# Kernel tuning notes

Hardware: AMD Instinct MI355X
Metric: run time of the kernel (lower is better)

## Reference

```python
import jax, jax.numpy as jnp
import numpy as np

B, C, H, W, O, K = 8, 3, 512, 512, 64, 9


def conv2d(x, w, b):
    # 3x3, stride 1, padding 1, NCHW/OIHW
    y = jax.lax.conv_general_dilated(
        x, w, window_strides=(1, 1), padding=[(1, 1), (1, 1)],
        dimension_numbers=('NCHW', 'OIHW', 'NCHW'))
    return y + b[None, :, None, None]


def setup_inputs() -> dict:
    key = jax.random.key(0)
    ks = jax.random.split(key, 6)
    x = jax.random.normal(ks[0], (B, C, H, W), jnp.float32)
    w_simple = jax.random.normal(ks[1], (O, C, 3, 3), jnp.float32) * 0.1
    w_off = jax.random.normal(ks[2], (2 * K, C, 3, 3), jnp.float32) * 0.05
    b_off = jax.random.normal(ks[3], (2 * K,), jnp.float32) * 0.1
    w_mask = jax.random.normal(ks[4], (K, C, 3, 3), jnp.float32) * 0.1
    b_mask = jax.random.normal(ks[5], (K,), jnp.float32) * 0.1
    return {'x': x, 'w_simple': w_simple, 'w_off': w_off, 'b_off': b_off,
            'w_mask': w_mask, 'b_mask': b_mask}


def deform_conv2d(x, offset, mask, weight):
    # x: [B,C,H,W]; offset: [B,2K,H,W] (dy,dx interleaved per tap);
    # mask: [B,K,H,W]; weight: [O,C,3,3]; stride 1, pad 1, dilation 1.
    off = offset.reshape(B, K, 2, H, W)
    dy, dx = off[:, :, 0], off[:, :, 1]          # [B,K,H,W]
    ki = (jnp.arange(K) // 3).astype(x.dtype)[None, :, None, None]
    kj = (jnp.arange(K) % 3).astype(x.dtype)[None, :, None, None]
    hh = jnp.arange(H, dtype=x.dtype)[None, None, :, None]
    ww = jnp.arange(W, dtype=x.dtype)[None, None, None, :]
    py = hh - 1.0 + ki + dy                       # sampling rows [B,K,H,W]
    px = ww - 1.0 + kj + dx                       # sampling cols [B,K,H,W]

    y0f = jnp.floor(py); x0f = jnp.floor(px)
    ty = py - y0f; tx = px - x0f                  # bilinear fractions
    y0 = y0f.astype(jnp.int32); x0 = x0f.astype(jnp.int32)

    def gather(yi, xi):
        # zero-padded gather of x at integer coords yi, xi -> [B,C,K,H,W]
        valid = ((yi >= 0) & (yi < H) & (xi >= 0) & (xi < W))
        yc = jnp.clip(yi, 0, H - 1)
        xc = jnp.clip(xi, 0, W - 1)
        lin = yc * W + xc                         # [B,K,H,W]
        def per_b(xb, linb):
            return xb.reshape(C, -1)[:, linb.reshape(-1)].reshape(C, K, H, W)
        vals = jax.vmap(per_b)(x, lin)
        return vals * valid[:, None].astype(x.dtype)

    v = (gather(y0, x0) * ((1 - ty) * (1 - tx))[:, None]
         + gather(y0, x0 + 1) * ((1 - ty) * tx)[:, None]
         + gather(y0 + 1, x0) * (ty * (1 - tx))[:, None]
         + gather(y0 + 1, x0 + 1) * (ty * tx)[:, None])  # [B,C,K,H,W]
    v = v * mask[:, None]                          # modulated samples
    return jnp.einsum('ock,bckhw->bohw', weight.reshape(O, C, K), v)


def reference(x, w_simple, w_off, b_off, w_mask, b_mask):
    offset = conv2d(x, w_off, b_off)
    mask = jax.nn.sigmoid(conv2d(x, w_mask, b_mask))
    return deform_conv2d(x, offset, mask, w_simple)
```

## Files before the change

### kernel.cpp

```cpp
#include <hip/hip_runtime.h>

#define BB 8
#define CC 3
#define HH 512
#define WW 512
#define OO 64
#define KK 9

__global__ __launch_bounds__(256, 4) void fused_deform_kernel(
    const float* __restrict__ x,
    const float* __restrict__ w_simple,
    const float* __restrict__ w_off,
    const float* __restrict__ b_off,
    const float* __restrict__ w_mask,
    const float* __restrict__ b_mask,
    float* __restrict__ out)
{
    __shared__ __align__(16) float s_woff[18 * 28];
    __shared__ __align__(16) float s_wmsk[9 * 28];
    __shared__ __align__(16) float s_w[64 * 28];
    __shared__ float s_boff[18];
    __shared__ float s_bmsk[9];

    const int tid = threadIdx.x;
    for (int t = tid; t < 18 * 28; t += 256) { int j = t / 28, i = t % 28; s_woff[t] = (i < 27) ? w_off[j * 27 + i] : 0.f; }
    for (int t = tid; t < 9 * 28; t += 256)  { int j = t / 28, i = t % 28; s_wmsk[t] = (i < 27) ? w_mask[j * 27 + i] : 0.f; }
    for (int t = tid; t < 64 * 28; t += 256) { int j = t / 28, i = t % 28; s_w[t]    = (i < 27) ? w_simple[j * 27 + i] : 0.f; }
    if (tid < 18) s_boff[tid] = b_off[tid];
    if (tid < 9)  s_bmsk[tid] = b_mask[tid];
    __syncthreads();

    const int bid = blockIdx.x;
    const int nbid = (bid & 7) * 1024 + (bid >> 3);

    const int idx = nbid * 256 + tid;
    const int w = idx & (WW - 1);
    const int h = (idx >> 9) & (HH - 1);
    const int b = idx >> 18;

    const float* xb = x + (size_t)b * CC * HH * WW;

    float nb[28];
    #pragma unroll
    for (int c = 0; c < CC; ++c) {
        const float* xc = xb + c * HH * WW;
        #pragma unroll
        for (int i = 0; i < 9; ++i) {
            int yy = h - 1 + i / 3;
            int xx = w - 1 + i % 3;
            float v = 0.f;
            if ((unsigned)yy < (unsigned)HH && (unsigned)xx < (unsigned)WW)
                v = xc[yy * WW + xx];
            nb[c * 9 + i] = v;
        }
    }
    nb[27] = 0.f;

    float offv[18];
    #pragma unroll
    for (int j = 0; j < 18; ++j) {
        float acc = s_boff[j];
        const float4* wp = (const float4*)(s_woff + j * 28);
        #pragma unroll
        for (int q = 0; q < 7; ++q) {
            float4 wq = wp[q];
            acc = fmaf(wq.x, nb[q * 4 + 0], acc);
            acc = fmaf(wq.y, nb[q * 4 + 1], acc);
            acc = fmaf(wq.z, nb[q * 4 + 2], acc);
            acc = fmaf(wq.w, nb[q * 4 + 3], acc);
        }
        offv[j] = acc;
    }

    float mval[9];
    #pragma unroll
    for (int j = 0; j < 9; ++j) {
        float acc = s_bmsk[j];
        const float4* wp = (const float4*)(s_wmsk + j * 28);
        #pragma unroll
        for (int q = 0; q < 7; ++q) {
            float4 wq = wp[q];
            acc = fmaf(wq.x, nb[q * 4 + 0], acc);
            acc = fmaf(wq.y, nb[q * 4 + 1], acc);
            acc = fmaf(wq.z, nb[q * 4 + 2], acc);
            acc = fmaf(wq.w, nb[q * 4 + 3], acc);
        }
        mval[j] = 1.f / (1.f + __expf(-acc));
    }

    float vv[28];
    vv[27] = 0.f;
    #pragma unroll
    for (int k = 0; k < 9; ++k) {
        float py = (float)(h - 1 + k / 3) + offv[2 * k + 0];
        float px = (float)(w - 1 + k % 3) + offv[2 * k + 1];
        float y0f = floorf(py);
        float x0f = floorf(px);
        float ty = py - y0f;
        float tx = px - x0f;
        int y0 = (int)y0f;
        int x0 = (int)x0f;
        int y1 = y0 + 1;
        int x1 = x0 + 1;
        bool vy0 = (unsigned)y0 < (unsigned)HH;
        bool vy1 = (unsigned)y1 < (unsigned)HH;
        bool vx0 = (unsigned)x0 < (unsigned)WW;
        bool vx1 = (unsigned)x1 < (unsigned)WW;
        int yc0 = min(max(y0, 0), HH - 1);
        int yc1 = min(max(y1, 0), HH - 1);
        int xc0 = min(max(x0, 0), WW - 1);
        int xc1 = min(max(x1, 0), WW - 1);
        int l00 = yc0 * WW + xc0;
        int l01 = yc0 * WW + xc1;
        int l10 = yc1 * WW + xc0;
        int l11 = yc1 * WW + xc1;
        float mk = mval[k];
        float w00 = (vy0 && vx0) ? (1.f - ty) * (1.f - tx) * mk : 0.f;
        float w01 = (vy0 && vx1) ? (1.f - ty) * tx * mk : 0.f;
        float w10 = (vy1 && vx0) ? ty * (1.f - tx) * mk : 0.f;
        float w11 = (vy1 && vx1) ? ty * tx * mk : 0.f;
        #pragma unroll
        for (int c = 0; c < CC; ++c) {
            const float* xc = xb + c * HH * WW;
            float s;
            s = w00 * xc[l00];
            s = fmaf(w01, xc[l01], s);
            s = fmaf(w10, xc[l10], s);
            s = fmaf(w11, xc[l11], s);
            vv[c * 9 + k] = s;
        }
    }

    const size_t obase = (size_t)b * OO * HH * WW + (size_t)h * WW + w;
    #pragma unroll 4
    for (int o = 0; o < OO; ++o) {
        float acc = 0.f;
        const float4* wp = (const float4*)(s_w + o * 28);
        #pragma unroll
        for (int q = 0; q < 7; ++q) {
            float4 wq = wp[q];
            acc = fmaf(wq.x, vv[q * 4 + 0], acc);
            acc = fmaf(wq.y, vv[q * 4 + 1], acc);
            acc = fmaf(wq.z, vv[q * 4 + 2], acc);
            acc = fmaf(wq.w, vv[q * 4 + 3], acc);
        }
        __builtin_nontemporal_store(acc, &out[obase + (size_t)o * HH * WW]);
    }
}

extern "C" void kernel_launch(void* const* d_in, const int* in_sizes, int n_in,
                              void* d_out, int out_size, void* d_ws, size_t ws_size,
                              hipStream_t stream) {
    const float* x        = (const float*)d_in[0];
    const float* w_simple = (const float*)d_in[1];
    const float* w_off    = (const float*)d_in[2];
    const float* b_off    = (const float*)d_in[3];
    const float* w_mask   = (const float*)d_in[4];
    const float* b_mask   = (const float*)d_in[5];
    float* out = (float*)d_out;

    const int total = BB * HH * WW;
    const int block = 256;
    const int grid = total / block;
    fused_deform_kernel<<<grid, block, 0, stream>>>(x, w_simple, w_off, b_off, w_mask, b_mask, out);
}
```

Before: 660.2 us.

## Compute output channel contraction with split-bf16 MFMA via per-wave LDS staging

Replaces the per-thread scalar 64x27 FMA loop for the final output projection with MFMA 16x16x32 bf16 instructions. Both weights and sampled values are split into hi/lo bf16 pairs, and three MFMAs approximate fp32 accuracy. Per-pixel samples are staged through per-wave LDS so they can be rearranged into the MFMA operand layout. The change also swaps the sigmoid divide for a hardware reciprocal and lowers launch bounds to account for the added LDS and register use. The split-bf16 scheme drops the lo*lo term, which slightly reduces precision, and the added LDS traffic costs some occupancy.

```diff
diff --git a/kernel.cpp b/kernel.cpp
--- a/kernel.cpp
+++ b/kernel.cpp
@@ -1,4 +1,7 @@
 #include <hip/hip_runtime.h>
+
+typedef __attribute__((ext_vector_type(8))) short bf8v;
+typedef __attribute__((ext_vector_type(4))) float f4v;
 
 #define BB 8
 #define CC 3
@@ -6,8 +9,20 @@
 #define WW 512
 #define OO 64
 #define KK 9
-
-__global__ __launch_bounds__(256, 4) void fused_deform_kernel(
+#define HW (HH * WW)
+#define VBSTRIDE 176
+
+static __device__ __forceinline__ unsigned short f2bf(float f) {
+    unsigned u = __builtin_bit_cast(unsigned, f);
+    unsigned r = u + 0x7fffu + ((u >> 16) & 1u);
+    return (unsigned short)(r >> 16);
+}
+static __device__ __forceinline__ float bf2f(unsigned short h) {
+    unsigned u = ((unsigned)h) << 16;
+    return __builtin_bit_cast(float, u);
+}
+
+__global__ __launch_bounds__(256, 3) void fused_deform_kernel(
     const float* __restrict__ x,
     const float* __restrict__ w_simple,
     const float* __restrict__ w_off,
@@ -18,16 +33,36 @@
 {
     __shared__ __align__(16) float s_woff[18 * 28];
     __shared__ __align__(16) float s_wmsk[9 * 28];
-    __shared__ __align__(16) float s_w[64 * 28];
     __shared__ float s_boff[18];
     __shared__ float s_bmsk[9];
+    __shared__ __align__(16) unsigned char s_vb[4 * 64 * VBSTRIDE];
 
     const int tid = threadIdx.x;
+    const int lane = tid & 63;
+    const int wv = tid >> 6;
+
     for (int t = tid; t < 18 * 28; t += 256) { int j = t / 28, i = t % 28; s_woff[t] = (i < 27) ? w_off[j * 27 + i] : 0.f; }
     for (int t = tid; t < 9 * 28; t += 256)  { int j = t / 28, i = t % 28; s_wmsk[t] = (i < 27) ? w_mask[j * 27 + i] : 0.f; }
-    for (int t = tid; t < 64 * 28; t += 256) { int j = t / 28, i = t % 28; s_w[t]    = (i < 27) ? w_simple[j * 27 + i] : 0.f; }
     if (tid < 18) s_boff[tid] = b_off[tid];
     if (tid < 9)  s_bmsk[tid] = b_mask[tid];
+
+    bf8v wh[4], wl[4];
+    {
+        const int row = lane & 15;
+        const int ko = (lane >> 4) * 8;
+        #pragma unroll
+        for (int m = 0; m < 4; ++m) {
+            const float* ws = w_simple + (size_t)(m * 16 + row) * 27 + ko;
+            #pragma unroll
+            for (int j = 0; j < 8; ++j) {
+                float f = (ko + j < 27) ? ws[j] : 0.f;
+                unsigned short hh = f2bf(f);
+                unsigned short ll = f2bf(f - bf2f(hh));
+                wh[m][j] = (short)hh;
+                wl[m][j] = (short)ll;
+            }
+        }
+    }
     __syncthreads();
 
     const int bid = blockIdx.x;
@@ -38,12 +73,12 @@
     const int h = (idx >> 9) & (HH - 1);
     const int b = idx >> 18;
 
-    const float* xb = x + (size_t)b * CC * HH * WW;
+    const float* xb = x + (size_t)b * CC * HW;
 
     float nb[28];
     #pragma unroll
     for (int c = 0; c < CC; ++c) {
-        const float* xc = xb + c * HH * WW;
+        const float* xc = xb + c * HW;
         #pragma unroll
         for (int i = 0; i < 9; ++i) {
             int yy = h - 1 + i / 3;
@@ -85,11 +120,10 @@
             acc = fmaf(wq.z, nb[q * 4 + 2], acc);
             acc = fmaf(wq.w, nb[q * 4 + 3], acc);
         }
-        mval[j] = 1.f / (1.f + __expf(-acc));
-    }
-
-    float vv[28];
-    vv[27] = 0.f;
+        mval[j] = __builtin_amdgcn_rcpf(1.f + __expf(-acc));
+    }
+
+    float vv[27];
     #pragma unroll
     for (int k = 0; k < 9; ++k) {
         float py = (float)(h - 1 + k / 3) + offv[2 * k + 0];
@@ -121,7 +155,7 @@
         float w11 = (vy1 && vx1) ? ty * tx * mk : 0.f;
         #pragma unroll
         for (int c = 0; c < CC; ++c) {
-            const float* xc = xb + c * HH * WW;
+            const float* xc = xb + c * HW;
             float s;
             s = w00 * xc[l00];
             s = fmaf(w01, xc[l01], s);
@@ -131,20 +165,51 @@
         }
     }
 
-    const size_t obase = (size_t)b * OO * HH * WW + (size_t)h * WW + w;
-    #pragma unroll 4
-    for (int o = 0; o < OO; ++o) {
-        float acc = 0.f;
-        const float4* wp = (const float4*)(s_w + o * 28);
-        #pragma unroll
-        for (int q = 0; q < 7; ++q) {
-            float4 wq = wp[q];
-            acc = fmaf(wq.x, vv[q * 4 + 0], acc);
-            acc = fmaf(wq.y, vv[q * 4 + 1], acc);
-            acc = fmaf(wq.z, vv[q * 4 + 2], acc);
-            acc = fmaf(wq.w, vv[q * 4 + 3], acc);
-        }
-        __builtin_nontemporal_store(acc, &out[obase + (size_t)o * HH * WW]);
+    unsigned char* vb = s_vb + wv * (64 * VBSTRIDE);
+    {
+        unsigned hiw[16], low[16];
+        #pragma unroll
+        for (int i = 0; i < 16; ++i) {
+            float a = (2 * i < 27) ? vv[2 * i] : 0.f;
+            float c2 = (2 * i + 1 < 27) ? vv[2 * i + 1] : 0.f;
+            unsigned short ha = f2bf(a), hb = f2bf(c2);
+            unsigned short la = f2bf(a - bf2f(ha)), lb = f2bf(c2 - bf2f(hb));
+            hiw[i] = (unsigned)ha | ((unsigned)hb << 16);
+            low[i] = (unsigned)la | ((unsigned)lb << 16);
+        }
+        uint4* dh = (uint4*)(vb + lane * VBSTRIDE);
+        dh[0] = make_uint4(hiw[0], hiw[1], hiw[2], hiw[3]);
+        dh[1] = make_uint4(hiw[4], hiw[5], hiw[6], hiw[7]);
+        dh[2] = make_uint4(hiw[8], hiw[9], hiw[10], hiw[11]);
+        dh[3] = make_uint4(hiw[12], hiw[13], hiw[14], hiw[15]);
+        uint4* dl = (uint4*)(vb + lane * VBSTRIDE + 64);
+        dl[0] = make_uint4(low[0], low[1], low[2], low[3]);
+        dl[1] = make_uint4(low[4], low[5], low[6], low[7]);
+        dl[2] = make_uint4(low[8], low[9], low[10], low[11]);
+        dl[3] = make_uint4(low[12], low[13], low[14], low[15]);
+    }
+    asm volatile("s_waitcnt lgkmcnt(0)" ::: "memory");
+
+    const int wavecol = ((nbid & 1) << 8) + wv * 64;
+    const int kb16 = (lane >> 4) * 16;
+    float* obase = out + (size_t)b * OO * HW + (size_t)h * WW;
+    #pragma unroll
+    for (int g = 0; g < 4; ++g) {
+        const unsigned char* rs = vb + (size_t)(g * 16 + (lane & 15)) * VBSTRIDE + kb16;
+        bf8v bh = *(const bf8v*)rs;
+        bf8v bl = *(const bf8v*)(rs + 64);
+        float* op0 = obase + (wavecol + g * 16 + (lane & 15));
+        #pragma unroll
+        for (int m = 0; m < 4; ++m) {
+            f4v acc = {0.f, 0.f, 0.f, 0.f};
+            acc = __builtin_amdgcn_mfma_f32_16x16x32_bf16(wh[m], bl, acc, 0, 0, 0);
+            acc = __builtin_amdgcn_mfma_f32_16x16x32_bf16(wl[m], bh, acc, 0, 0, 0);
+            acc = __builtin_amdgcn_mfma_f32_16x16x32_bf16(wh[m], bh, acc, 0, 0, 0);
+            const int o0 = m * 16 + (lane >> 4) * 4;
+            #pragma unroll
+            for (int r = 0; r < 4; ++r)
+                __builtin_nontemporal_store(acc[r], op0 + (size_t)(o0 + r) * HW);
+        }
     }
 }
 
```

Result: slower. 848.5 us (+28.5%).
